# Optimization experiments

Hardware: AMD Instinct MI355X
Metric: run time of the kernel (lower is better)

The kernel has to match this reference:

```python
import jax, jax.numpy as jnp
import numpy as np

NODE_IN = 128
NODE_OUT = 128
LEAKY_SLOPE = 0.01  # torch nn.LeakyReLU default


def setup_inputs() -> dict:
    key = jax.random.key(0)
    k1, k2, k3, k4 = jax.random.split(key, 4)
    B, N = 64, 1024
    node_mat = jax.random.normal(k1, (B, N, NODE_IN), dtype=jnp.float32)
    adj_mat = jax.random.uniform(k2, (B, N, N), dtype=jnp.float32)
    # Linear(node_in_len, node_out_len): W [out, in], b [out] (torch default init style)
    bound = 1.0 / np.sqrt(NODE_IN)
    W = jax.random.uniform(k3, (NODE_OUT, NODE_IN), minval=-bound, maxval=bound, dtype=jnp.float32)
    b = jax.random.uniform(k4, (NODE_OUT,), minval=-bound, maxval=bound, dtype=jnp.float32)
    return {"node_mat": node_mat, "adj_mat": adj_mat, "W": W, "b": b}


def reference(node_mat, adj_mat, W, b):
    # n_neighbors[b,i] = sum_j adj[b,i,j]; diag(1/deg) @ adj == adj / deg (row-wise)
    deg = jnp.sum(adj_mat, axis=-1, keepdims=True)          # [B,N,1]
    norm_adj = adj_mat / deg                                 # [B,N,N]
    agg = jnp.einsum('bij,bjf->bif', norm_adj, node_mat)     # [B,N,Fin]
    out = jnp.einsum('bif,of->bio', agg, W) + b              # [B,N,Fout]
    return jnp.where(out >= 0, out, LEAKY_SLOPE * out)
```

## Files before the change

### kernel.cpp

```cpp
#include <hip/hip_runtime.h>
#include <hip/hip_bf16.h>


typedef __attribute__((ext_vector_type(8))) short bf16x8;
typedef __attribute__((ext_vector_type(4))) float f32x4;

__device__ __forceinline__ unsigned f2bf(float x) {
  unsigned u = __builtin_bit_cast(unsigned, x);
  u += 0x7FFFu + ((u >> 16) & 1u);
  return u >> 16;
}
__device__ __forceinline__ int f2bf2(float x, float y) {
  return (int)(f2bf(x) | (f2bf(y) << 16));
}

#define JPAD 136

__global__ __launch_bounds__(256) void k_ht(const float* __restrict__ node,
                                            const float* __restrict__ W,
                                            ushort* __restrict__ Ht) {
  __shared__ short nt[128 * JPAD];
  __shared__ short wt[128 * JPAD];
  const int b = blockIdx.y, jt = blockIdx.x, t = threadIdx.x;
  const float4* nbase = (const float4*)(node + (size_t)(b * 1024 + jt * 128) * 128);
  const float4* wbase = (const float4*)W;

  #pragma unroll
  for (int p = 0; p < 16; p++) {
    int idx = t + 256 * p;
    int r = idx >> 5, c4 = idx & 31;
    float4 v = nbase[idx];
    int2 s; s.x = f2bf2(v.x, v.y); s.y = f2bf2(v.z, v.w);
    *(int2*)&nt[r * JPAD + c4 * 4] = s;
    float4 wv = wbase[idx];
    int2 sw; sw.x = f2bf2(wv.x, wv.y); sw.y = f2bf2(wv.z, wv.w);
    *(int2*)&wt[r * JPAD + c4 * 4] = sw;
  }
  __syncthreads();

  const int lane = t & 63, wid = t >> 6;
  const int q = lane >> 4, r = lane & 15;
  const int wm = wid & 1, wn = wid >> 1;
  f32x4 acc[4][4] = {};
  #pragma unroll
  for (int ks = 0; ks < 4; ks++) {
    bf16x8 af[4], bg[4];
    #pragma unroll
    for (int mi = 0; mi < 4; mi++)
      af[mi] = *(const bf16x8*)&nt[(wm * 64 + mi * 16 + r) * JPAD + ks * 32 + q * 8];
    #pragma unroll
    for (int ni = 0; ni < 4; ni++)
      bg[ni] = *(const bf16x8*)&wt[(wn * 64 + ni * 16 + r) * JPAD + ks * 32 + q * 8];
    #pragma unroll
    for (int mi = 0; mi < 4; mi++)
      #pragma unroll
      for (int ni = 0; ni < 4; ni++)
        acc[mi][ni] = __builtin_amdgcn_mfma_f32_16x16x32_bf16(af[mi], bg[ni], acc[mi][ni], 0, 0, 0);
  }
  __syncthreads();

  #pragma unroll
  for (int mi = 0; mi < 4; mi++)
    #pragma unroll
    for (int ni = 0; ni < 4; ni++)
      #pragma unroll
      for (int v = 0; v < 4; v++) {
        int j = wm * 64 + mi * 16 + q * 4 + v;
        int o = wn * 64 + ni * 16 + r;
        nt[o * JPAD + j] = (short)f2bf(acc[mi][ni][v]);
      }
  __syncthreads();
  {
    int o = t >> 1, half = t & 1;
    const int4* src = (const int4*)&nt[o * JPAD + half * 64];
    int4* dst = (int4*)(Ht + (size_t)b * 131072 + (size_t)o * 1024 + jt * 128 + half * 64);
    #pragma unroll
    for (int i = 0; i < 8; i++) dst[i] = src[i];
  }
}

__global__ __launch_bounds__(256) void k_main(const float* __restrict__ adj,
                                              const ushort* __restrict__ Ht,
                                              const float* __restrict__ bias,
                                              float* __restrict__ out) {
  const int b = blockIdx.y, it = blockIdx.x, t = threadIdx.x;
  const int lane = t & 63, wid = t >> 6;
  const int q = lane >> 4, r = lane & 15;
  const int i0 = it * 64 + wid * 16;
  const float4* ap = (const float4*)(adj + (size_t)(b * 1024 + i0 + r) * 1024);
  const int4* hb = (const int4*)(Ht + (size_t)b * 131072) + r * 128;

  f32x4 acc[8] = {};
  float rs = 0.f;

  float4 a0 = ap[q * 2], a1 = ap[q * 2 + 1], a2 = ap[q * 2 + 8], a3 = ap[q * 2 + 9];

  #pragma unroll 1
  for (int kt = 0; kt < 16; kt++) {
    int4 bv[8];
    #pragma unroll
    for (int ni = 0; ni < 8; ni++) bv[ni] = hb[ni * 2048 + kt * 8 + q];

    union { bf16x8 v; int i[4]; } u0, u1;
    u0.i[0] = f2bf2(a0.x, a0.y); u0.i[1] = f2bf2(a0.z, a0.w);
    u0.i[2] = f2bf2(a1.x, a1.y); u0.i[3] = f2bf2(a1.z, a1.w);
    u1.i[0] = f2bf2(a2.x, a2.y); u1.i[1] = f2bf2(a2.z, a2.w);
    u1.i[2] = f2bf2(a3.x, a3.y); u1.i[3] = f2bf2(a3.z, a3.w);
    rs += (a0.x + a0.y + a0.z + a0.w) + (a1.x + a1.y + a1.z + a1.w)
        + (a2.x + a2.y + a2.z + a2.w) + (a3.x + a3.y + a3.z + a3.w);

    const int nb = (kt < 15 ? kt + 1 : 15) * 16 + q * 2;
    float4 n0 = ap[nb], n1 = ap[nb + 1], n2 = ap[nb + 8], n3 = ap[nb + 9];

    #pragma unroll
    for (int ni = 0; ni < 8; ni++)
      acc[ni] = __builtin_amdgcn_mfma_f32_16x16x32_bf16(
          u0.v, __builtin_bit_cast(bf16x8, bv[ni]), acc[ni], 0, 0, 0);

    #pragma unroll
    for (int ni = 0; ni < 8; ni++) bv[ni] = hb[ni * 2048 + kt * 8 + 4 + q];
    #pragma unroll
    for (int ni = 0; ni < 8; ni++)
      acc[ni] = __builtin_amdgcn_mfma_f32_16x16x32_bf16(
          u1.v, __builtin_bit_cast(bf16x8, bv[ni]), acc[ni], 0, 0, 0);

    a0 = n0; a1 = n1; a2 = n2; a3 = n3;
  }

  rs += __shfl_xor(rs, 16);
  rs += __shfl_xor(rs, 32);

  float* obase = out + (size_t)(b * 1024 + i0) * 128;
  #pragma unroll
  for (int v = 0; v < 4; v++) {
    const float rd = 1.0f / __shfl(rs, q * 4 + v);
    const int i = q * 4 + v;
    #pragma unroll
    for (int ni = 0; ni < 8; ni++) {
      float val = acc[ni][v] * rd + bias[ni * 16 + r];
      val = val >= 0.0f ? val : 0.01f * val;
      obase[(size_t)i * 128 + ni * 16 + r] = val;
    }
  }
}

__global__ __launch_bounds__(256) void k_fallback(const float* __restrict__ node,
                                                  const float* __restrict__ adj,
                                                  const float* __restrict__ W,
                                                  const float* __restrict__ bias,
                                                  float* __restrict__ out) {
  __shared__ float red[256];
  __shared__ float agg[128];
  const int b = blockIdx.y, i = blockIdx.x, t = threadIdx.x;
  const float* arow = adj + (size_t)(b * 1024 + i) * 1024;
  float s = 0.f;
  for (int j = t; j < 1024; j += 256) s += arow[j];
  red[t] = s;
  __syncthreads();
  if (t < 128) red[t] += red[t + 128];
  __syncthreads();
  if (t < 64) {
    float v2 = red[t] + red[t + 64];
    #pragma unroll
    for (int off = 32; off; off >>= 1) v2 += __shfl_down(v2, off);
    if (t == 0) red[0] = v2;
  }
  __syncthreads();
  const float rdeg = 1.0f / red[0];
  const int f = t & 127, half = t >> 7;
  const float* nb = node + (size_t)b * 1024 * 128;
  float a = 0.f;
  for (int j = half * 512; j < half * 512 + 512; j++)
    a += arow[j] * nb[(size_t)j * 128 + f];
  __syncthreads();
  if (half == 0) agg[f] = a;
  __syncthreads();
  if (half == 1) agg[f] += a;
  __syncthreads();
  if (t < 128) {
    const float* wr = W + t * 128;
    float o = 0.f;
    for (int f2 = 0; f2 < 128; f2++) o += agg[f2] * wr[f2];
    o = o * rdeg + bias[t];
    out[(size_t)(b * 1024 + i) * 128 + t] = o >= 0.f ? o : 0.01f * o;
  }
}

extern "C" void kernel_launch(void* const* d_in, const int* in_sizes, int n_in,
                              void* d_out, int out_size, void* d_ws, size_t ws_size,
                              hipStream_t stream) {
  const float* node = (const float*)d_in[0];
  const float* adj  = (const float*)d_in[1];
  const float* W    = (const float*)d_in[2];
  const float* bias = (const float*)d_in[3];
  float* out = (float*)d_out;
  const size_t ht_bytes = (size_t)64 * 128 * 1024 * 2;
  if (ws_size >= ht_bytes) {
    ushort* Ht = (ushort*)d_ws;
    k_ht<<<dim3(8, 64), 256, 0, stream>>>(node, W, Ht);
    k_main<<<dim3(16, 64), 256, 0, stream>>>(adj, Ht, bias, out);
  } else {
    k_fallback<<<dim3(1024, 64), 256, 0, stream>>>(node, adj, W, bias, out);
  }
}
```

Baseline: 469.8 us.

## Stage Ht tiles in swizzled, double-buffered LDS via direct global-to-LDS loads

In the main aggregation kernel, the four waves of a block previously each fetched the same transformed-feature tile (Ht) from global memory. They now cooperatively load it once per k-step into a double-buffered LDS tile, using direct global-to-LDS 16-byte loads with an XOR swizzle to avoid bank conflicts. This cuts redundant L2/global traffic for Ht by roughly the number of waves, and the next tile is prefetched while the current one is consumed. In exchange it adds a block-wide barrier every iteration and 32 KB of LDS per block, which may lower occupancy.

```diff
diff --git a/kernel.cpp b/kernel.cpp
--- a/kernel.cpp
+++ b/kernel.cpp
@@ -12,6 +12,12 @@
 }
 __device__ __forceinline__ int f2bf2(float x, float y) {
   return (int)(f2bf(x) | (f2bf(y) << 16));
+}
+
+__device__ __forceinline__ void gload_lds16(const void* g, void* l) {
+  __builtin_amdgcn_global_load_lds(
+      (const __attribute__((address_space(1))) unsigned int*)g,
+      (__attribute__((address_space(3))) unsigned int*)l, 16, 0, 0);
 }
 
 #define JPAD 136
@@ -83,23 +89,38 @@
                                               const ushort* __restrict__ Ht,
                                               const float* __restrict__ bias,
                                               float* __restrict__ out) {
+  __shared__ short hbuf[2][128 * 64];
   const int b = blockIdx.y, it = blockIdx.x, t = threadIdx.x;
   const int lane = t & 63, wid = t >> 6;
   const int q = lane >> 4, r = lane & 15;
   const int i0 = it * 64 + wid * 16;
   const float4* ap = (const float4*)(adj + (size_t)(b * 1024 + i0 + r) * 1024);
-  const int4* hb = (const int4*)(Ht + (size_t)b * 131072) + r * 128;
+
+  const int o_l = wid * 32 + (lane >> 3);
+  const int cchunk = (lane & 7) ^ ((lane >> 3) & 7);
+  const ushort* gsrc = Ht + (size_t)b * 131072 + (size_t)o_l * 1024 + cchunk * 8;
+
+  const int boff0 = r * 128 + (((0 * 4 + q) ^ (r & 7)) << 4);
+  const int boff1 = r * 128 + (((1 * 4 + q) ^ (r & 7)) << 4);
 
   f32x4 acc[8] = {};
   float rs = 0.f;
 
+  #pragma unroll
+  for (int p = 0; p < 4; p++)
+    gload_lds16(gsrc + (size_t)p * 8192, &hbuf[0][(wid * 32 + 8 * p) * 64]);
   float4 a0 = ap[q * 2], a1 = ap[q * 2 + 1], a2 = ap[q * 2 + 8], a3 = ap[q * 2 + 9];
-
+  __syncthreads();
+
+  int c = 0;
   #pragma unroll 1
   for (int kt = 0; kt < 16; kt++) {
-    int4 bv[8];
-    #pragma unroll
-    for (int ni = 0; ni < 8; ni++) bv[ni] = hb[ni * 2048 + kt * 8 + q];
+    if (kt < 15) {
+      #pragma unroll
+      for (int p = 0; p < 4; p++)
+        gload_lds16(gsrc + (size_t)p * 8192 + (kt + 1) * 64,
+                    &hbuf[c ^ 1][(wid * 32 + 8 * p) * 64]);
+    }
 
     union { bf16x8 v; int i[4]; } u0, u1;
     u0.i[0] = f2bf2(a0.x, a0.y); u0.i[1] = f2bf2(a0.z, a0.w);
@@ -112,19 +133,24 @@
     const int nb = (kt < 15 ? kt + 1 : 15) * 16 + q * 2;
     float4 n0 = ap[nb], n1 = ap[nb + 1], n2 = ap[nb + 8], n3 = ap[nb + 9];
 
+    const char* hb = (const char*)&hbuf[c][0];
+    int4 bv[8];
+    #pragma unroll
+    for (int ni = 0; ni < 8; ni++) bv[ni] = *(const int4*)(hb + boff0 + ni * 2048);
     #pragma unroll
     for (int ni = 0; ni < 8; ni++)
       acc[ni] = __builtin_amdgcn_mfma_f32_16x16x32_bf16(
           u0.v, __builtin_bit_cast(bf16x8, bv[ni]), acc[ni], 0, 0, 0);
-
-    #pragma unroll
-    for (int ni = 0; ni < 8; ni++) bv[ni] = hb[ni * 2048 + kt * 8 + 4 + q];
+    #pragma unroll
+    for (int ni = 0; ni < 8; ni++) bv[ni] = *(const int4*)(hb + boff1 + ni * 2048);
     #pragma unroll
     for (int ni = 0; ni < 8; ni++)
       acc[ni] = __builtin_amdgcn_mfma_f32_16x16x32_bf16(
           u1.v, __builtin_bit_cast(bf16x8, bv[ni]), acc[ni], 0, 0, 0);
 
     a0 = n0; a1 = n1; a2 = n2; a3 = n3;
+    __syncthreads();
+    c ^= 1;
   }
 
   rs += __shfl_xor(rs, 16);
```

After: 411.9 us. -12.3%, faster.
